# Optimization experiments

Measured on AMD Instinct MI355X. Metric: run time of the kernel, lower is better.

The kernel has to match this reference:

```python
import jax, jax.numpy as jnp
import numpy as np

IN_DIM = 1024
EMBED = 512
N_PATCH = 8191  # +1 cls token -> n=8192, divisible by k-chunk 512
K_CHUNK = 512
NUM_CLASSES = 2


def setup_inputs() -> dict:
    key = jax.random.key(0)
    ks = jax.random.split(key, 16)
    g = lambda i, shape, scale=0.02: jax.random.normal(ks[i], shape, dtype=jnp.float32) * scale
    return {
        "x": jax.random.normal(ks[0], (1, N_PATCH, IN_DIM), dtype=jnp.float32),
        "W1": g(1, (IN_DIM, EMBED)), "b1": jnp.zeros((EMBED,), jnp.float32),
        "cls_token": jax.random.normal(ks[2], (1, 1, EMBED), dtype=jnp.float32),
        "Wq": g(3, (EMBED, EMBED)), "bq": jnp.zeros((EMBED,), jnp.float32),
        "Wk": g(4, (EMBED, EMBED)), "bk": jnp.zeros((EMBED,), jnp.float32),
        "Wv": g(5, (EMBED, EMBED)), "bv": jnp.zeros((EMBED,), jnp.float32),
        "Wo": g(6, (EMBED, EMBED)), "bo": jnp.zeros((EMBED,), jnp.float32),
        "ln_g": jnp.ones((EMBED,), jnp.float32), "ln_b": jnp.zeros((EMBED,), jnp.float32),
        "Wc": g(7, (EMBED, NUM_CLASSES)), "bc": jnp.zeros((NUM_CLASSES,), jnp.float32),
    }


def reference(x, W1, b1, cls_token, Wq, bq, Wk, bk, Wv, bv, Wo, bo, ln_g, ln_b, Wc, bc):
    # feature_proj: Linear -> ReLU (dropout=0 -> identity)
    h = jax.nn.relu(x @ W1 + b1)                       # [b, N, E]
    b_, _, e = h.shape
    h = jnp.concatenate([jnp.broadcast_to(cls_token, (b_, 1, e)), h], axis=1)  # prepend cls
    b, n, d = h.shape                                   # n = 8192 > 5000 path
    q = h @ Wq + bq
    k = h @ Wk + bk
    v = h @ Wv + bv
    scores = jnp.einsum("bqd,bkd->bqk", q, k) / (d ** 0.5)  # [b, n, n]
    # n>5000 branch: softmax within each K_CHUNK slice of keys, then re-softmax over full n
    w = jax.nn.softmax(scores.reshape(b, n, n // K_CHUNK, K_CHUNK), axis=-1).reshape(b, n, n)
    w = jax.nn.softmax(w, axis=-1)
    attn = jnp.einsum("bqk,bkd->bqd", w, v)
    h = h + attn @ Wo + bo                              # residual
    # LayerNorm (eps=1e-5)
    mu = h.mean(-1, keepdims=True)
    var = ((h - mu) ** 2).mean(-1, keepdims=True)
    hn = (h - mu) / jnp.sqrt(var + 1e-5) * ln_g + ln_b
    cls_feat = hn[:, 0, :]
    logits = cls_feat @ Wc + bc                         # [b, num_classes]
    return logits
```

## Files before the change

kernel.cpp:

```cpp
#include <hip/hip_runtime.h>
#include <math.h>

typedef __attribute__((ext_vector_type(8))) short bf16x8;
typedef __attribute__((ext_vector_type(4))) float f32x4;

#define AS1(p) ((__attribute__((address_space(1))) void*)(uintptr_t)(p))
#define AS3(p) ((__attribute__((address_space(3))) void*)(p))

static __device__ __forceinline__ unsigned short f2bf(float f) {
    unsigned int u = __float_as_uint(f);
    unsigned int r = (u + 0x7fffu + ((u >> 16) & 1u)) >> 16;
    return (unsigned short)r;
}
static __device__ __forceinline__ unsigned int cvtpk_bf16(float lo, float hi) {
    unsigned int r;
    asm("v_cvt_pk_bf16_f32 %0, %1, %2" : "=v"(r) : "v"(lo), "v"(hi));
    return r;
}

#define NPATCH 8191
#define NTOK   8192
#define INDIM  1024
#define EMBED  512

__global__ void k_pre(const float* __restrict__ W1, unsigned short* __restrict__ w1t,
                      const float* __restrict__ cls, const float* __restrict__ Wq,
                      const float* __restrict__ bq, const float* __restrict__ bv,
                      const float* __restrict__ bo,
                      float* __restrict__ q0, float* __restrict__ h_full,
                      float* __restrict__ svec, float* __restrict__ attn0,
                      float* __restrict__ r0, float* __restrict__ scores) {
    const int b = blockIdx.x;
    const int t = threadIdx.x;
    if (b < 512) {
        __shared__ float tile[32][33];
        const int bk = b >> 4;
        const int bn = b & 15;
        const int r  = t >> 3;
        const int c4 = (t & 7) * 4;
        float4 v = *(const float4*)(W1 + (size_t)(bk * 32 + r) * EMBED + bn * 32 + c4);
        tile[r][c4 + 0] = v.x; tile[r][c4 + 1] = v.y; tile[r][c4 + 2] = v.z; tile[r][c4 + 3] = v.w;
        __syncthreads();
        ushort4 o;
        o.x = f2bf(tile[c4 + 0][r]); o.y = f2bf(tile[c4 + 1][r]);
        o.z = f2bf(tile[c4 + 2][r]); o.w = f2bf(tile[c4 + 3][r]);
        *(ushort4*)(w1t + (size_t)(bn * 32 + r) * INDIM + bk * 32 + c4) = o;
    } else if (t < 128) {
        const int d = (b - 512) * 128 + t;
        float acc = 0.f;
        for (int in = 0; in < EMBED; ++in)
            acc = fmaf(cls[in], Wq[in * EMBED + d], acc);
        q0[d]     = acc + bq[d];
        h_full[d] = cls[d];
        svec[d]   = 0.f;
        attn0[d]  = bv[d];
        r0[d]     = cls[d] + bo[d];
        #pragma unroll
        for (int i = 0; i < 16; ++i) scores[d * 16 + i] = 0.f;
    }
}

__global__ void k_u(const float* __restrict__ Wk, const float* __restrict__ q0,
                    float* __restrict__ u) {
    const int wave = blockIdx.x * 4 + (threadIdx.x >> 6);
    const int lane = threadIdx.x & 63;
    const float4* q4 = (const float4*)q0;
    float4 qa = q4[lane * 2], qb = q4[lane * 2 + 1];
    for (int rr = 0; rr < 4; ++rr) {
        const int row = wave * 4 + rr;
        const float4* wr = (const float4*)(Wk + (size_t)row * EMBED);
        float4 a = wr[lane * 2], b = wr[lane * 2 + 1];
        float acc = a.x*qa.x + a.y*qa.y + a.z*qa.z + a.w*qa.w
                  + b.x*qb.x + b.y*qb.y + b.z*qb.z + b.w*qb.w;
        for (int off = 32; off; off >>= 1) acc += __shfl_down(acc, off);
        if (lane == 0) u[row] = acc;
    }
}

__global__ __launch_bounds__(256) void k_gemm(const float* __restrict__ x,
                                              const unsigned short* __restrict__ w1t,
                                              const float* __restrict__ b1,
                                              const float* __restrict__ u,
                                              float* __restrict__ h_full,
                                              float* __restrict__ scores) {
    __shared__ unsigned short As[2][64 * 64];
    __shared__ unsigned short Bs[2][64 * 64];
    const int tid  = threadIdx.x;
    const int wave = tid >> 6;
    const int lane = tid & 63;
    const int bid  = blockIdx.x;
    const int tile = ((bid & 7) << 7) | (bid >> 3);
    const int gm   = tile >> 3;
    const int gn   = tile & 7;
    const int wr   = wave >> 1, wc = wave & 1;
    const int fr   = lane & 15, fq = lane >> 4;

    int dstA[2];
    size_t srcA[2];
    #pragma unroll
    for (int oi = 0; oi < 2; ++oi) {
        const int row = oi * 32 + (tid >> 3), slot = tid & 7;
        dstA[oi] = row * 64 + (slot ^ (row & 7)) * 8;
        const int xrow = min(gm * 64 + row, NPATCH - 1);
        srcA[oi] = (size_t)xrow * INDIM + slot * 8;
    }
    size_t srcB[2];
    int ldsB[2];
    #pragma unroll
    for (int i = 0; i < 2; ++i) {
        const int rbase = wave * 16 + i * 8;
        const int r = rbase + (lane >> 3), s = lane & 7;
        srcB[i] = (size_t)(gn * 64 + r) * INDIM + (s ^ (r & 7)) * 8;
        ldsB[i] = rbase * 64;
    }

    f32x4 acc[2][2] = {};
    float4 ar[2][2];

    int aoff[2], boff[2];
    #pragma unroll
    for (int mi = 0; mi < 2; ++mi) {
        const int row = wr * 32 + mi * 16 + fr;
        aoff[mi] = row * 64 + ((row & 7) ^ fq) * 8;
        const int col = wc * 32 + mi * 16 + fr;
        boff[mi] = col * 64 + ((col & 7) ^ fq) * 8;
    }

#define LOADB(buf, k0) do { \
    _Pragma("unroll") \
    for (int i = 0; i < 2; ++i) \
        __builtin_amdgcn_global_load_lds(AS1(w1t + srcB[i] + (k0)), \
                                         AS3(&Bs[buf][ldsB[i]]), 16, 0, 0); \
    } while (0)

#define LOADA(k0) do { \
    _Pragma("unroll") \
    for (int oi = 0; oi < 2; ++oi) { \
        const float4* pa = (const float4*)(x + srcA[oi] + (k0)); \
        ar[oi][0] = pa[0]; ar[oi][1] = pa[1]; \
    } } while (0)

#define WRITEA(buf) do { \
    _Pragma("unroll") \
    for (int oi = 0; oi < 2; ++oi) { \
        int4 aw; \
        aw.x = (int)cvtpk_bf16(ar[oi][0].x, ar[oi][0].y); \
        aw.y = (int)cvtpk_bf16(ar[oi][0].z, ar[oi][0].w); \
        aw.z = (int)cvtpk_bf16(ar[oi][1].x, ar[oi][1].y); \
        aw.w = (int)cvtpk_bf16(ar[oi][1].z, ar[oi][1].w); \
        *(int4*)&As[buf][dstA[oi]] = aw; \
    } } while (0)

    LOADB(0, 0);
    LOADA(0);
    WRITEA(0);
    __syncthreads();

    int cur = 0;
    for (int t = 0; t < 16; ++t) {
        if (t < 15) {
            LOADB(cur ^ 1, (t + 1) * 64);
            LOADA((t + 1) * 64);
        }
        #pragma unroll
        for (int kk = 0; kk < 2; ++kk) {
            bf16x8 af[2], bfr[2];
            #pragma unroll
            for (int mi = 0; mi < 2; ++mi)
                af[mi] = *(const bf16x8*)&As[cur][aoff[mi] ^ (kk * 32)];
            #pragma unroll
            for (int ni = 0; ni < 2; ++ni)
                bfr[ni] = *(const bf16x8*)&Bs[cur][boff[ni] ^ (kk * 32)];
            #pragma unroll
            for (int mi = 0; mi < 2; ++mi)
                #pragma unroll
                for (int ni = 0; ni < 2; ++ni)
                    acc[mi][ni] = __builtin_amdgcn_mfma_f32_16x16x32_bf16(af[mi], bfr[ni], acc[mi][ni], 0, 0, 0);
        }
        if (t < 15) WRITEA(cur ^ 1);
        __syncthreads();
        cur ^= 1;
    }

    float uv[2], bvv[2];
    #pragma unroll
    for (int ni = 0; ni < 2; ++ni) {
        const int col = gn * 64 + wc * 32 + ni * 16 + fr;
        uv[ni]  = u[col];
        bvv[ni] = b1[col];
    }
    #pragma unroll
    for (int mi = 0; mi < 2; ++mi) {
        #pragma unroll
        for (int rr = 0; rr < 4; ++rr) {
            const int a = gm * 64 + wr * 32 + mi * 16 + fq * 4 + rr;
            if (a < NPATCH) {
                float sc = 0.f;
                #pragma unroll
                for (int ni = 0; ni < 2; ++ni) {
                    const int col = gn * 64 + wc * 32 + ni * 16 + fr;
                    float v = fmaxf(acc[mi][ni][rr] + bvv[ni], 0.f);
                    h_full[(size_t)(a + 1) * EMBED + col] = v;
                    sc = fmaf(v, uv[ni], sc);
                }
                sc += __shfl_xor(sc, 1);
                sc += __shfl_xor(sc, 2);
                sc += __shfl_xor(sc, 4);
                sc += __shfl_xor(sc, 8);
                if (fr == 0) atomicAdd(&scores[a + 1], sc);
            }
        }
    }
#undef LOADB
#undef LOADA
#undef WRITEA
}

__global__ void k_softmax(const float* __restrict__ scores, const float* __restrict__ h_full,
                          const float* __restrict__ u, float* __restrict__ wts) {
    __shared__ float redA[16], redB[16];
    __shared__ float s0sh;
    const int t = threadIdx.x, wv = t >> 6, lane = t & 63;
    const float rs = 0.04419417382415922f;

    if (wv == 0) {
        const float4* hr = (const float4*)h_full;
        const float4* u4 = (const float4*)u;
        float4 a = hr[lane * 2], b = hr[lane * 2 + 1];
        float4 qa = u4[lane * 2], qb = u4[lane * 2 + 1];
        float acc = a.x*qa.x + a.y*qa.y + a.z*qa.z + a.w*qa.w
                  + b.x*qb.x + b.y*qb.y + b.z*qb.z + b.w*qb.w;
        for (int off = 32; off; off >>= 1) acc += __shfl_down(acc, off);
        if (lane == 0) s0sh = acc * rs;
    }
    __syncthreads();

    const float4* s4 = (const float4*)scores;
    float4 a = s4[2 * t], b = s4[2 * t + 1];
    float v[8] = {a.x*rs, a.y*rs, a.z*rs, a.w*rs, b.x*rs, b.y*rs, b.z*rs, b.w*rs};
    if (t == 0) v[0] = s0sh;

    float mx = v[0];
    #pragma unroll
    for (int j = 1; j < 8; ++j) mx = fmaxf(mx, v[j]);
    for (int off = 32; off; off >>= 1) mx = fmaxf(mx, __shfl_xor(mx, off));
    float sm = 0.f;
    #pragma unroll
    for (int j = 0; j < 8; ++j) { v[j] = expf(v[j] - mx); sm += v[j]; }
    for (int off = 32; off; off >>= 1) sm += __shfl_xor(sm, off);
    float inv = 1.f / sm;
    #pragma unroll
    for (int j = 0; j < 8; ++j) v[j] *= inv;

    float m2 = v[0];
    #pragma unroll
    for (int j = 1; j < 8; ++j) m2 = fmaxf(m2, v[j]);
    for (int off = 32; off; off >>= 1) m2 = fmaxf(m2, __shfl_xor(m2, off));
    if (lane == 0) redA[wv] = m2;
    __syncthreads();
    float gm = redA[0];
    for (int i = 1; i < 16; ++i) gm = fmaxf(gm, redA[i]);
    float s2 = 0.f;
    #pragma unroll
    for (int j = 0; j < 8; ++j) { v[j] = expf(v[j] - gm); s2 += v[j]; }
    for (int off = 32; off; off >>= 1) s2 += __shfl_xor(s2, off);
    if (lane == 0) redB[wv] = s2;
    __syncthreads();
    float gs = 0.f;
    for (int i = 0; i < 16; ++i) gs += redB[i];
    float gi = 1.f / gs;
    float4 o1 = {v[0] * gi, v[1] * gi, v[2] * gi, v[3] * gi};
    float4 o2 = {v[4] * gi, v[5] * gi, v[6] * gi, v[7] * gi};
    float4* w4 = (float4*)wts;
    w4[2 * t] = o1; w4[2 * t + 1] = o2;
}

__global__ void k_wsum(const float* __restrict__ h_full, const float* __restrict__ wts,
                       float* __restrict__ svec) {
    const int b = blockIdx.x, t = threadIdx.x;
    float a0 = 0.f, a1 = 0.f;
    const int j0 = b * 32;
    for (int j = j0; j < j0 + 32; ++j) {
        const float wj = wts[j];
        const float* hr = h_full + (size_t)j * EMBED;
        a0 = fmaf(wj, hr[t], a0);
        a1 = fmaf(wj, hr[t + 256], a1);
    }
    atomicAdd(&svec[t], a0);
    atomicAdd(&svec[t + 256], a1);
}

__global__ void k_attn0(const float* __restrict__ svec, const float* __restrict__ Wv,
                        float* __restrict__ attn0) {
    const int b = blockIdx.x, t = threadIdx.x;
    float a0 = 0.f, a1 = 0.f;
    const int e0 = b * 16;
    for (int e = e0; e < e0 + 16; ++e) {
        const float s = svec[e];
        const float* wr = Wv + (size_t)e * EMBED;
        a0 = fmaf(s, wr[t], a0);
        a1 = fmaf(s, wr[t + 256], a1);
    }
    atomicAdd(&attn0[t], a0);
    atomicAdd(&attn0[t + 256], a1);
}

__global__ void k_r0(const float* __restrict__ attn0, const float* __restrict__ Wo,
                     float* __restrict__ r0) {
    const int b = blockIdx.x, t = threadIdx.x;
    float a0 = 0.f, a1 = 0.f;
    const int e0 = b * 16;
    for (int e = e0; e < e0 + 16; ++e) {
        const float s = attn0[e];
        const float* wr = Wo + (size_t)e * EMBED;
        a0 = fmaf(s, wr[t], a0);
        a1 = fmaf(s, wr[t + 256], a1);
    }
    atomicAdd(&r0[t], a0);
    atomicAdd(&r0[t + 256], a1);
}

__global__ void k_final(const float* __restrict__ r0, const float* __restrict__ ln_g,
                        const float* __restrict__ ln_b, const float* __restrict__ Wc,
                        const float* __restrict__ bc, float* __restrict__ out) {
    __shared__ float red[8];
    const int t = threadIdx.x, wv = t >> 6, lane = t & 63;
    const float x = r0[t];

    float sm = x;
    for (int off = 32; off; off >>= 1) sm += __shfl_down(sm, off);
    if (lane == 0) red[wv] = sm;
    __syncthreads();
    float mu = 0.f;
    for (int i = 0; i < 8; ++i) mu += red[i];
    mu *= (1.f / 512.f);
    const float dx = x - mu;

    __syncthreads();
    float q = dx * dx;
    for (int off = 32; off; off >>= 1) q += __shfl_down(q, off);
    if (lane == 0) red[wv] = q;
    __syncthreads();
    float var = 0.f;
    for (int i = 0; i < 8; ++i) var += red[i];
    var *= (1.f / 512.f);

    const float hn = dx / sqrtf(var + 1e-5f) * ln_g[t] + ln_b[t];
    float p0 = hn * Wc[2 * t];
    float p1 = hn * Wc[2 * t + 1];

    __syncthreads();
    for (int off = 32; off; off >>= 1) p0 += __shfl_down(p0, off);
    if (lane == 0) red[wv] = p0;
    __syncthreads();
    if (t == 0) {
        float tot = 0.f;
        for (int i = 0; i < 8; ++i) tot += red[i];
        out[0] = tot + bc[0];
    }
    __syncthreads();
    for (int off = 32; off; off >>= 1) p1 += __shfl_down(p1, off);
    if (lane == 0) red[wv] = p1;
    __syncthreads();
    if (t == 0) {
        float tot = 0.f;
        for (int i = 0; i < 8; ++i) tot += red[i];
        out[1] = tot + bc[1];
    }
}

extern "C" void kernel_launch(void* const* d_in, const int* in_sizes, int n_in,
                              void* d_out, int out_size, void* d_ws, size_t ws_size,
                              hipStream_t stream) {
    const float* x    = (const float*)d_in[0];
    const float* W1   = (const float*)d_in[1];
    const float* b1   = (const float*)d_in[2];
    const float* cls  = (const float*)d_in[3];
    const float* Wq   = (const float*)d_in[4];
    const float* bq   = (const float*)d_in[5];
    const float* Wk   = (const float*)d_in[6];
    const float* bk   = (const float*)d_in[7];   (void)bk;
    const float* Wv   = (const float*)d_in[8];
    const float* bv   = (const float*)d_in[9];
    const float* Wo   = (const float*)d_in[10];
    const float* bo   = (const float*)d_in[11];
    const float* ln_g = (const float*)d_in[12];
    const float* ln_b = (const float*)d_in[13];
    const float* Wc   = (const float*)d_in[14];
    const float* bc   = (const float*)d_in[15];
    float* out = (float*)d_out;

    char* ws = (char*)d_ws;
    unsigned short* w1t    = (unsigned short*)(ws);
    float*          h_full = (float*)(ws + 1048576);
    float*          scores = (float*)(ws + 17825792);
    float*          wts    = (float*)(ws + 17858560);
    float*          q0     = (float*)(ws + 17891328);
    float*          u      = (float*)(ws + 17893376);
    float*          svec   = (float*)(ws + 17895424);
    float*          attn0  = (float*)(ws + 17897472);
    float*          r0     = (float*)(ws + 17899520);

    k_pre     <<<516, 256, 0, stream>>>(W1, w1t, cls, Wq, bq, bv, bo,
                                        q0, h_full, svec, attn0, r0, scores);
    k_u       <<<32,  256, 0, stream>>>(Wk, q0, u);
    k_gemm    <<<1024,256, 0, stream>>>(x, w1t, b1, u, h_full, scores);
    k_softmax <<<1,  1024, 0, stream>>>(scores, h_full, u, wts);
    k_wsum    <<<256, 256, 0, stream>>>(h_full, wts, svec);
    k_attn0   <<<32,  256, 0, stream>>>(svec, Wv, attn0);
    k_r0      <<<32,  256, 0, stream>>>(attn0, Wo, r0);
    k_final   <<<1,   512, 0, stream>>>(r0, ln_g, ln_b, Wc, bc, out);
}
```

Measured before the change: 175.0 us.

## Pre-convert x to bf16 and enlarge GEMM tiles to 128x128 with async LDS loads

The fp32 x is converted to bf16 once in the preprocessing kernel and stored in a padded workspace buffer. The GEMM now loads both operands straight into LDS with global_load_lds and uses 128x128x128 tiles, giving each wave a 4x4 MFMA block instead of 2x2. The aim is more data reuse per tile and no register round-trip or conversion inside the GEMM loop. In exchange the workspace grows, an extra 16 MB bf16 copy is written and read back, the grid shrinks to 256 blocks, and each block now needs 128 KB of LDS.

```diff
diff --git a/kernel.cpp b/kernel.cpp
--- a/kernel.cpp
+++ b/kernel.cpp
@@ -12,18 +12,14 @@
     unsigned int r = (u + 0x7fffu + ((u >> 16) & 1u)) >> 16;
     return (unsigned short)r;
 }
-static __device__ __forceinline__ unsigned int cvtpk_bf16(float lo, float hi) {
-    unsigned int r;
-    asm("v_cvt_pk_bf16_f32 %0, %1, %2" : "=v"(r) : "v"(lo), "v"(hi));
-    return r;
-}
 
 #define NPATCH 8191
 #define NTOK   8192
 #define INDIM  1024
 #define EMBED  512
 
-__global__ void k_pre(const float* __restrict__ W1, unsigned short* __restrict__ w1t,
+__global__ void k_pre(const float* __restrict__ x, unsigned short* __restrict__ xb,
+                      const float* __restrict__ W1, unsigned short* __restrict__ w1t,
                       const float* __restrict__ cls, const float* __restrict__ Wq,
                       const float* __restrict__ bq, const float* __restrict__ bv,
                       const float* __restrict__ bo,
@@ -32,10 +28,24 @@
                       float* __restrict__ r0, float* __restrict__ scores) {
     const int b = blockIdx.x;
     const int t = threadIdx.x;
-    if (b < 512) {
+    if (b < 2048) {
+        const int NV = NPATCH * INDIM / 4;
+        const int NT = NTOK   * INDIM / 4;
+        for (int i = b * 256 + t; i < NT; i += 2048 * 256) {
+            ushort4 o;
+            if (i < NV) {
+                float4 v = ((const float4*)x)[i];
+                o.x = f2bf(v.x); o.y = f2bf(v.y); o.z = f2bf(v.z); o.w = f2bf(v.w);
+            } else {
+                o.x = 0; o.y = 0; o.z = 0; o.w = 0;
+            }
+            ((ushort4*)xb)[i] = o;
+        }
+    } else if (b < 2560) {
         __shared__ float tile[32][33];
-        const int bk = b >> 4;
-        const int bn = b & 15;
+        const int bb = b - 2048;
+        const int bk = bb >> 4;
+        const int bn = bb & 15;
         const int r  = t >> 3;
         const int c4 = (t & 7) * 4;
         float4 v = *(const float4*)(W1 + (size_t)(bk * 32 + r) * EMBED + bn * 32 + c4);
@@ -46,7 +56,7 @@
         o.z = f2bf(tile[c4 + 2][r]); o.w = f2bf(tile[c4 + 3][r]);
         *(ushort4*)(w1t + (size_t)(bn * 32 + r) * INDIM + bk * 32 + c4) = o;
     } else if (t < 128) {
-        const int d = (b - 512) * 128 + t;
+        const int d = (b - 2560) * 128 + t;
         float acc = 0.f;
         for (int in = 0; in < EMBED; ++in)
             acc = fmaf(cls[in], Wq[in * EMBED + d], acc);
@@ -77,128 +87,101 @@
     }
 }
 
-__global__ __launch_bounds__(256) void k_gemm(const float* __restrict__ x,
+__global__ __launch_bounds__(256) void k_gemm(const unsigned short* __restrict__ xb,
                                               const unsigned short* __restrict__ w1t,
                                               const float* __restrict__ b1,
                                               const float* __restrict__ u,
                                               float* __restrict__ h_full,
                                               float* __restrict__ scores) {
-    __shared__ unsigned short As[2][64 * 64];
-    __shared__ unsigned short Bs[2][64 * 64];
+    __shared__ __align__(16) unsigned short As[2][128 * 128];
+    __shared__ __align__(16) unsigned short Bs[2][128 * 128];
     const int tid  = threadIdx.x;
     const int wave = tid >> 6;
     const int lane = tid & 63;
     const int bid  = blockIdx.x;
-    const int tile = ((bid & 7) << 7) | (bid >> 3);
-    const int gm   = tile >> 3;
-    const int gn   = tile & 7;
+    const int rg   = (bid & 7) | ((bid >> 5) << 3);
+    const int cg   = (bid >> 3) & 3;
     const int wr   = wave >> 1, wc = wave & 1;
     const int fr   = lane & 15, fq = lane >> 4;
 
-    int dstA[2];
-    size_t srcA[2];
-    #pragma unroll
-    for (int oi = 0; oi < 2; ++oi) {
-        const int row = oi * 32 + (tid >> 3), slot = tid & 7;
-        dstA[oi] = row * 64 + (slot ^ (row & 7)) * 8;
-        const int xrow = min(gm * 64 + row, NPATCH - 1);
-        srcA[oi] = (size_t)xrow * INDIM + slot * 8;
-    }
-    size_t srcB[2];
-    int ldsB[2];
-    #pragma unroll
-    for (int i = 0; i < 2; ++i) {
-        const int rbase = wave * 16 + i * 8;
-        const int r = rbase + (lane >> 3), s = lane & 7;
-        srcB[i] = (size_t)(gn * 64 + r) * INDIM + (s ^ (r & 7)) * 8;
-        ldsB[i] = rbase * 64;
-    }
-
-    f32x4 acc[2][2] = {};
-    float4 ar[2][2];
-
-    int aoff[2], boff[2];
-    #pragma unroll
-    for (int mi = 0; mi < 2; ++mi) {
-        const int row = wr * 32 + mi * 16 + fr;
-        aoff[mi] = row * 64 + ((row & 7) ^ fq) * 8;
-        const int col = wc * 32 + mi * 16 + fr;
-        boff[mi] = col * 64 + ((col & 7) ^ fq) * 8;
-    }
-
-#define LOADB(buf, k0) do { \
+    size_t srcA[8], srcB[8];
+    int dstc[8];
+    #pragma unroll
+    for (int i = 0; i < 8; ++i) {
+        const int c0  = (i * 4 + wave) * 64;
+        const int c   = c0 + lane;
+        const int row = c >> 4, koct = c & 15;
+        const int kg  = koct ^ (row & 7);
+        dstc[i] = c0 * 8;
+        srcA[i] = (size_t)(rg * 128 + row) * INDIM + kg * 8;
+        srcB[i] = (size_t)(cg * 128 + row) * INDIM + kg * 8;
+    }
+
+    f32x4 acc[4][4] = {};
+
+    int aoff[4], boff[4];
+    #pragma unroll
+    for (int mi = 0; mi < 4; ++mi) {
+        const int row = wr * 64 + mi * 16 + fr;
+        aoff[mi] = row * 128 + ((fq ^ (row & 7)) * 8);
+        const int col = wc * 64 + mi * 16 + fr;
+        boff[mi] = col * 128 + ((fq ^ (col & 7)) * 8);
+    }
+
+#define STAGE(buf, k0) do { \
     _Pragma("unroll") \
-    for (int i = 0; i < 2; ++i) \
+    for (int i = 0; i < 8; ++i) \
+        __builtin_amdgcn_global_load_lds(AS1(xb + srcA[i] + (k0)), \
+                                         AS3(&As[buf][dstc[i]]), 16, 0, 0); \
+    _Pragma("unroll") \
+    for (int i = 0; i < 8; ++i) \
         __builtin_amdgcn_global_load_lds(AS1(w1t + srcB[i] + (k0)), \
-                                         AS3(&Bs[buf][ldsB[i]]), 16, 0, 0); \
+                                         AS3(&Bs[buf][dstc[i]]), 16, 0, 0); \
     } while (0)
 
-#define LOADA(k0) do { \
-    _Pragma("unroll") \
-    for (int oi = 0; oi < 2; ++oi) { \
-        const float4* pa = (const float4*)(x + srcA[oi] + (k0)); \
-        ar[oi][0] = pa[0]; ar[oi][1] = pa[1]; \
-    } } while (0)
-
-#define WRITEA(buf) do { \
-    _Pragma("unroll") \
-    for (int oi = 0; oi < 2; ++oi) { \
-        int4 aw; \
-        aw.x = (int)cvtpk_bf16(ar[oi][0].x, ar[oi][0].y); \
-        aw.y = (int)cvtpk_bf16(ar[oi][0].z, ar[oi][0].w); \
-        aw.z = (int)cvtpk_bf16(ar[oi][1].x, ar[oi][1].y); \
-        aw.w = (int)cvtpk_bf16(ar[oi][1].z, ar[oi][1].w); \
-        *(int4*)&As[buf][dstA[oi]] = aw; \
-    } } while (0)
-
-    LOADB(0, 0);
-    LOADA(0);
-    WRITEA(0);
+    STAGE(0, 0);
     __syncthreads();
 
     int cur = 0;
-    for (int t = 0; t < 16; ++t) {
-        if (t < 15) {
-            LOADB(cur ^ 1, (t + 1) * 64);
-            LOADA((t + 1) * 64);
-        }
+    for (int kt = 0; kt < 8; ++kt) {
+        if (kt < 7) STAGE(cur ^ 1, (kt + 1) * 128);
         #pragma unroll
-        for (int kk = 0; kk < 2; ++kk) {
-            bf16x8 af[2], bfr[2];
+        for (int kk = 0; kk < 4; ++kk) {
+            bf16x8 af[4], bf[4];
             #pragma unroll
-            for (int mi = 0; mi < 2; ++mi)
+            for (int mi = 0; mi < 4; ++mi)
                 af[mi] = *(const bf16x8*)&As[cur][aoff[mi] ^ (kk * 32)];
             #pragma unroll
-            for (int ni = 0; ni < 2; ++ni)
-                bfr[ni] = *(const bf16x8*)&Bs[cur][boff[ni] ^ (kk * 32)];
+            for (int ni = 0; ni < 4; ++ni)
+                bf[ni] = *(const bf16x8*)&Bs[cur][boff[ni] ^ (kk * 32)];
             #pragma unroll
-            for (int mi = 0; mi < 2; ++mi)
+            for (int mi = 0; mi < 4; ++mi)
                 #pragma unroll
-                for (int ni = 0; ni < 2; ++ni)
-                    acc[mi][ni] = __builtin_amdgcn_mfma_f32_16x16x32_bf16(af[mi], bfr[ni], acc[mi][ni], 0, 0, 0);
+                for (int ni = 0; ni < 4; ++ni)
+                    acc[mi][ni] = __builtin_amdgcn_mfma_f32_16x16x32_bf16(af[mi], bf[ni], acc[mi][ni], 0, 0, 0);
         }
-        if (t < 15) WRITEA(cur ^ 1);
         __syncthreads();
         cur ^= 1;
     }
-
-    float uv[2], bvv[2];
-    #pragma unroll
-    for (int ni = 0; ni < 2; ++ni) {
-        const int col = gn * 64 + wc * 32 + ni * 16 + fr;
+#undef STAGE
+
+    float uv[4], bvv[4];
+    #pragma unroll
+    for (int ni = 0; ni < 4; ++ni) {
+        const int col = cg * 128 + wc * 64 + ni * 16 + fr;
         uv[ni]  = u[col];
         bvv[ni] = b1[col];
     }
     #pragma unroll
-    for (int mi = 0; mi < 2; ++mi) {
+    for (int mi = 0; mi < 4; ++mi) {
         #pragma unroll
         for (int rr = 0; rr < 4; ++rr) {
-            const int a = gm * 64 + wr * 32 + mi * 16 + fq * 4 + rr;
+            const int a = rg * 128 + wr * 64 + mi * 16 + fq * 4 + rr;
             if (a < NPATCH) {
                 float sc = 0.f;
                 #pragma unroll
-                for (int ni = 0; ni < 2; ++ni) {
-                    const int col = gn * 64 + wc * 32 + ni * 16 + fr;
+                for (int ni = 0; ni < 4; ++ni) {
+                    const int col = cg * 128 + wc * 64 + ni * 16 + fr;
                     float v = fmaxf(acc[mi][ni][rr] + bvv[ni], 0.f);
                     h_full[(size_t)(a + 1) * EMBED + col] = v;
                     sc = fmaf(v, uv[ni], sc);
@@ -211,9 +194,6 @@
             }
         }
     }
-#undef LOADB
-#undef LOADA
-#undef WRITEA
 }
 
 __global__ void k_softmax(const float* __restrict__ scores, const float* __restrict__ h_full,
@@ -391,20 +371,21 @@
     float* out = (float*)d_out;
 
     char* ws = (char*)d_ws;
-    unsigned short* w1t    = (unsigned short*)(ws);
-    float*          h_full = (float*)(ws + 1048576);
-    float*          scores = (float*)(ws + 17825792);
-    float*          wts    = (float*)(ws + 17858560);
-    float*          q0     = (float*)(ws + 17891328);
-    float*          u      = (float*)(ws + 17893376);
-    float*          svec   = (float*)(ws + 17895424);
-    float*          attn0  = (float*)(ws + 17897472);
-    float*          r0     = (float*)(ws + 17899520);
-
-    k_pre     <<<516, 256, 0, stream>>>(W1, w1t, cls, Wq, bq, bv, bo,
-                                        q0, h_full, svec, attn0, r0, scores);
+    unsigned short* xb     = (unsigned short*)(ws);
+    unsigned short* w1t    = (unsigned short*)(ws + 16777216);
+    float*          h_full = (float*)(ws + 17825792);
+    float*          scores = (float*)(ws + 34603008);
+    float*          wts    = (float*)(ws + 34635776);
+    float*          q0     = (float*)(ws + 34668544);
+    float*          u      = (float*)(ws + 34670592);
+    float*          svec   = (float*)(ws + 34672640);
+    float*          attn0  = (float*)(ws + 34674688);
+    float*          r0     = (float*)(ws + 34676736);
+
+    k_pre     <<<2564, 256, 0, stream>>>(x, xb, W1, w1t, cls, Wq, bq, bv, bo,
+                                         q0, h_full, svec, attn0, r0, scores);
     k_u       <<<32,  256, 0, stream>>>(Wk, q0, u);
-    k_gemm    <<<1024,256, 0, stream>>>(x, w1t, b1, u, h_full, scores);
+    k_gemm    <<<256, 256, 0, stream>>>(xb, w1t, b1, u, h_full, scores);
     k_softmax <<<1,  1024, 0, stream>>>(scores, h_full, u, wts);
     k_wsum    <<<256, 256, 0, stream>>>(h_full, wts, svec);
     k_attn0   <<<32,  256, 0, stream>>>(svec, Wv, attn0);
```

Result: slower. 180.1 us (+2.9%).
